# Kernel optimization log

Measured on AMD Instinct MI355X. Metric: run time of the kernel, lower is better.

Reference implementation:

```python
import jax, jax.numpy as jnp
import numpy as np

B, N, DIM = 32, 1024, 768
H, S, D = 16, 4, 64  # num_heads, num_subheads (L=H*S=64), attn_dim


def setup_inputs() -> dict:
    key = jax.random.key(0)
    k1, k2, k3, k4 = jax.random.split(key, 4)
    x = jax.random.normal(k1, (B, N, DIM), dtype=jnp.float32)
    eos_indices = jax.random.randint(k2, (B,), 0, N)
    # q_emb: original shape (1,H,S,1,D); singleton dims dropped -> (H,S,D)
    q_emb = jax.random.normal(k3, (H, S, D), dtype=jnp.float32)
    # k Linear(dim -> H*D), xavier-uniform weight, zero bias (share_kv: v == k)
    limit = float(np.sqrt(6.0 / (DIM + H * D)))
    Wk = jax.random.uniform(k4, (DIM, H * D), dtype=jnp.float32, minval=-limit, maxval=limit)
    bk = jnp.zeros((H * D,), dtype=jnp.float32)
    return {"x": x, "eos_indices": eos_indices, "q_emb": q_emb, "Wk": Wk, "bk": bk}


def reference(x, eos_indices, q_emb, Wk, bk):
    # x: (B,N,dim); shared k/v projection -> (B,N,H,D)
    kv = (x @ Wk + bk).reshape(x.shape[0], x.shape[1], H, D)
    scale = D ** -0.5
    # Avoid the torch expand over subheads: contract directly.
    # logits: (B,H,S,N)
    logits = jnp.einsum("hsd,bnhd->bhsn", q_emb * scale, kv)
    # eos masking: positions strictly after eos index are masked out
    mask = jnp.arange(x.shape[1])[None, None, None, :] > eos_indices[:, None, None, None]
    logits = jnp.where(mask, -jnp.inf, logits)
    attn = jax.nn.softmax(logits, axis=-1)
    # weighted sum over N -> (B,H,S,D) -> (B,L,D)
    out = jnp.einsum("bhsn,bnhd->bhsd", attn, kv)
    return out.reshape(x.shape[0], H * S, D)
```

## Files before the change

kernel.cpp:

```cpp
#include <hip/hip_runtime.h>
#include <hip/hip_bf16.h>
#include <stdint.h>

typedef float  f32x4  __attribute__((ext_vector_type(4)));
typedef __bf16 bf16x4 __attribute__((ext_vector_type(4)));
typedef __bf16 bf16x8 __attribute__((ext_vector_type(8)));
typedef unsigned int u32x2 __attribute__((ext_vector_type(2)));
typedef unsigned int u32x4 __attribute__((ext_vector_type(4)));

#define AS1 __attribute__((address_space(1)))
#define AS3 __attribute__((address_space(3)))

__device__ __forceinline__ void async_load16(const void* g, void* lds) {
    __builtin_amdgcn_global_load_lds((const AS1 unsigned int*)g,
                                     (AS3 unsigned int*)lds, 16, 0, 0);
}

__global__ __launch_bounds__(256) void qw_kernel(const float* __restrict__ q_emb,
                                                 const float* __restrict__ wk,
                                                 __bf16* __restrict__ qwT) {
    __shared__ float qlds[256];
    __shared__ float part[4096];
    const int t = threadIdx.x;
    const int kc = blockIdx.x;
    const int h  = blockIdx.y;
    const int k0 = kc * 64;
    qlds[t] = q_emb[h * 256 + t] * 0.125f;
    __syncthreads();
    const int dseg = t & 15;
    const int krow = t >> 4;
#pragma unroll
    for (int i = 0; i < 4; ++i) {
        const int k = i * 16 + krow;
        f32x4 wv = *(const f32x4*)&wk[(size_t)(k0 + k) * 1024 + h * 64 + dseg * 4];
#pragma unroll
        for (int s = 0; s < 4; ++s) {
            float p = qlds[s * 64 + dseg * 4 + 0] * wv[0]
                    + qlds[s * 64 + dseg * 4 + 1] * wv[1]
                    + qlds[s * 64 + dseg * 4 + 2] * wv[2]
                    + qlds[s * 64 + dseg * 4 + 3] * wv[3];
            part[k * 64 + s * 16 + dseg] = p;
        }
    }
    __syncthreads();
    const int k = t >> 2, s = t & 3;
    const float* pp = &part[k * 64 + s * 16];
    float sum = 0.f;
#pragma unroll
    for (int j = 0; j < 16; ++j) sum += pp[j];
    qwT[(h * 4 + s) * 768 + k0 + k] = (__bf16)sum;
}

__global__ __launch_bounds__(512) void logits_kernel(const float* __restrict__ x,
                                                     const __bf16* __restrict__ qwT,
                                                     float* __restrict__ Lg) {
    __shared__ char smem[49152];
    char* Bl = smem;
    char* Al = smem + 16384;
    const int t = threadIdx.x, l = t & 63, w = t >> 6;
    const int m0 = blockIdx.x * 128;
    const int bb = m0 >> 10, n0 = m0 & 1023;
    const int wrA = (w >> 1) * 32;
    const int wcB = (w & 1) * 32;

    f32x4 acc[2][2];
#pragma unroll
    for (int i = 0; i < 2; ++i)
#pragma unroll
        for (int j = 0; j < 2; ++j) acc[i][j] = (f32x4)0.f;

    const int Bcol = t >> 3, Bseg = t & 7;
    const __bf16* qsrc = qwT + Bcol * 768 + (Bseg ^ (Bcol & 7)) * 8;
    const int Arow0 = t >> 4;
    const int Aseg = t & 15;

    f32x4 av[4];
    async_load16(qsrc, Bl + t * 16);
#pragma unroll
    for (int i = 0; i < 4; ++i)
        av[i] = *(const f32x4*)&x[(size_t)(m0 + i * 32 + Arow0) * 768 + Aseg * 4];
#pragma unroll
    for (int i = 0; i < 4; ++i) {
        const int row = i * 32 + Arow0;
        bf16x4 vv = {(__bf16)av[i][0], (__bf16)av[i][1], (__bf16)av[i][2], (__bf16)av[i][3]};
        *(bf16x4*)(Al + ((row * 128 + Aseg * 8) ^ ((row & 7) << 4))) = vv;
    }
    asm volatile("s_waitcnt vmcnt(0)" ::: "memory");
    __syncthreads();

    int buf = 0;
    for (int step = 0; step < 12; ++step) {
        const int nbuf = buf ^ 1;
        const bool more = (step + 1) < 12;
        if (more) {
            const int kt = (step + 1) * 64;
            async_load16(qsrc + kt, Bl + nbuf * 8192 + t * 16);
#pragma unroll
            for (int i = 0; i < 4; ++i)
                av[i] = *(const f32x4*)&x[(size_t)(m0 + i * 32 + Arow0) * 768 + kt + Aseg * 4];
        }
#pragma unroll
        for (int kh = 0; kh < 2; ++kh) {
            const int u = kh * 4 + (l >> 4);
            bf16x8 af[2], bfr[2];
#pragma unroll
            for (int i = 0; i < 2; ++i) {
                const int row = wrA + i * 16 + (l & 15);
                af[i] = *(const bf16x8*)(Al + buf * 16384 +
                                         ((row * 128 + u * 16) ^ ((row & 7) << 4)));
            }
#pragma unroll
            for (int j = 0; j < 2; ++j) {
                const int col = wcB + j * 16 + (l & 15);
                bfr[j] = *(const bf16x8*)(Bl + buf * 8192 +
                                          ((col * 128 + u * 16) ^ ((col & 7) << 4)));
            }
#pragma unroll
            for (int i = 0; i < 2; ++i)
#pragma unroll
                for (int j = 0; j < 2; ++j)
                    acc[i][j] = __builtin_amdgcn_mfma_f32_16x16x32_bf16(
                        af[i], bfr[j], acc[i][j], 0, 0, 0);
        }
        if (more) {
#pragma unroll
            for (int i = 0; i < 4; ++i) {
                const int row = i * 32 + Arow0;
                bf16x4 vv = {(__bf16)av[i][0], (__bf16)av[i][1], (__bf16)av[i][2], (__bf16)av[i][3]};
                *(bf16x4*)(Al + nbuf * 16384 + ((row * 128 + Aseg * 8) ^ ((row & 7) << 4))) = vv;
            }
        }
        asm volatile("s_waitcnt vmcnt(0)" ::: "memory");
        __syncthreads();
        buf = nbuf;
    }

#pragma unroll
    for (int i = 0; i < 2; ++i)
#pragma unroll
        for (int j = 0; j < 2; ++j) {
            const int hs = wcB + j * 16 + (l & 15);
            const int nb = wrA + i * 16 + (l >> 4) * 4;
            *(f32x4*)(smem + ((hs * 512 + nb * 4) ^ ((hs & 7) << 4))) = acc[i][j];
        }
    __syncthreads();
    const int hs = t >> 3;
#pragma unroll
    for (int i = 0; i < 4; ++i) {
        const int seg = (t & 7) + i * 8;
        f32x4 v = *(const f32x4*)(smem + ((hs * 512 + seg * 16) ^ ((hs & 7) << 4)));
        *(f32x4*)&Lg[(size_t)bb * 65536 + hs * 1024 + n0 + seg * 4] = v;
    }
}

__global__ __launch_bounds__(256) void softmax_kernel(const float* __restrict__ Lg,
                                                      const int* __restrict__ eos_idx,
                                                      __bf16* __restrict__ P) {
    const int t = threadIdx.x, l = t & 63, s = t >> 6;
    const int b = blockIdx.x >> 4, h = blockIdx.x & 15;
    const int eos = eos_idx[b];
    const size_t base = (size_t)(b * 64 + h * 4 + s) * 1024;
    f32x4 v[4];
    float mx = -INFINITY;
#pragma unroll
    for (int i = 0; i < 4; ++i) {
        v[i] = *(const f32x4*)&Lg[base + i * 256 + l * 4];
#pragma unroll
        for (int j = 0; j < 4; ++j) {
            if (i * 256 + l * 4 + j > eos) v[i][j] = -INFINITY;
            mx = fmaxf(mx, v[i][j]);
        }
    }
#pragma unroll
    for (int off = 32; off; off >>= 1) mx = fmaxf(mx, __shfl_xor(mx, off));
    float sum = 0.f;
#pragma unroll
    for (int i = 0; i < 4; ++i)
#pragma unroll
        for (int j = 0; j < 4; ++j) {
            const float p = __expf(v[i][j] - mx);
            v[i][j] = p;
            sum += p;
        }
#pragma unroll
    for (int off = 32; off; off >>= 1) sum += __shfl_xor(sum, off);
    const float inv = 1.0f / sum;
#pragma unroll
    for (int i = 0; i < 4; ++i) {
        bf16x4 pk = {(__bf16)(v[i][0] * inv), (__bf16)(v[i][1] * inv),
                     (__bf16)(v[i][2] * inv), (__bf16)(v[i][3] * inv)};
        *(bf16x4*)&P[base + i * 256 + l * 4] = pk;
    }
}

__global__ __launch_bounds__(256) void pv_kernel(const float* __restrict__ x,
                                                 const __bf16* __restrict__ P,
                                                 float* __restrict__ y) {
    __shared__ char smem[32768];
    char* Pl = smem;
    char* Xl = smem + 16384;
    const int t = threadIdx.x, l = t & 63, w = t >> 6;
    const int vid = (blockIdx.x & 7) * 48 + (blockIdx.x >> 3);
    const int b = vid / 12, kc = vid % 12;
    const int k0 = kc * 64;
    const int wrA = (w >> 1) * 32, wcB = (w & 1) * 32;
    const __bf16* Pb = P + (size_t)b * 65536;
    const float* xb = x + (size_t)b * 786432 + k0 + l;
    const int fK = ((l & 7) << 4) | (((l >> 3) & 1) << 3);

    f32x4 acc[2][2];
#pragma unroll
    for (int i = 0; i < 2; ++i)
#pragma unroll
        for (int j = 0; j < 2; ++j) acc[i][j] = (f32x4)0.f;

    const int Prow = t >> 3;
    const int Pseg = t & 7;

    float xv[16];
#pragma unroll
    for (int ii = 0; ii < 2; ++ii) {
        const int row = ii * 32 + Prow;
        async_load16(Pb + row * 1024 + (Pseg ^ (row & 7)) * 8, Pl + ii * 4096 + t * 16);
    }
#pragma unroll
    for (int i = 0; i < 4; ++i)
#pragma unroll
        for (int j = 0; j < 4; ++j)
            xv[i * 4 + j] = xb[(size_t)(i * 16 + w * 4 + j) * 768];
#pragma unroll
    for (int i = 0; i < 4; ++i) {
        bf16x4 vv = {(__bf16)xv[i * 4 + 0], (__bf16)xv[i * 4 + 1],
                     (__bf16)xv[i * 4 + 2], (__bf16)xv[i * 4 + 3]};
        const int nb2 = (i * 16 + w * 4) * 2;
        *(bf16x4*)(Xl + ((l * 128 + nb2) ^ fK)) = vv;
    }
    asm volatile("s_waitcnt vmcnt(0)" ::: "memory");
    __syncthreads();

    int buf = 0;
    for (int step = 0; step < 16; ++step) {
        const int nbuf = buf ^ 1;
        const bool more = (step + 1) < 16;
        if (more) {
            const int nt = (step + 1) * 64;
#pragma unroll
            for (int ii = 0; ii < 2; ++ii) {
                const int row = ii * 32 + Prow;
                async_load16(Pb + row * 1024 + nt + (Pseg ^ (row & 7)) * 8,
                             Pl + nbuf * 8192 + ii * 4096 + t * 16);
            }
#pragma unroll
            for (int i = 0; i < 4; ++i)
#pragma unroll
                for (int j = 0; j < 4; ++j)
                    xv[i * 4 + j] = xb[(size_t)(nt + i * 16 + w * 4 + j) * 768];
        }
#pragma unroll
        for (int kh = 0; kh < 2; ++kh) {
            const int u = kh * 4 + (l >> 4);
            bf16x8 af[2], bfr[2];
#pragma unroll
            for (int i = 0; i < 2; ++i) {
                const int row = wrA + i * 16 + (l & 15);
                af[i] = *(const bf16x8*)(Pl + buf * 8192 +
                                         ((row * 128 + u * 16) ^ ((row & 7) << 4)));
            }
#pragma unroll
            for (int j = 0; j < 2; ++j) {
                const int kcol = wcB + j * 16 + (l & 15);
                const int fKc = ((kcol & 7) << 4) | (((kcol >> 3) & 1) << 3);
                const int addrA = kcol * 128 + kh * 64 + (l >> 4) * 16;
                u32x2 lo = *(const u32x2*)(Xl + buf * 8192 + (addrA ^ fKc));
                u32x2 hi = *(const u32x2*)(Xl + buf * 8192 + ((addrA + 8) ^ fKc));
                u32x4 uu = {lo[0], lo[1], hi[0], hi[1]};
                bfr[j] = __builtin_bit_cast(bf16x8, uu);
            }
#pragma unroll
            for (int i = 0; i < 2; ++i)
#pragma unroll
                for (int j = 0; j < 2; ++j)
                    acc[i][j] = __builtin_amdgcn_mfma_f32_16x16x32_bf16(
                        af[i], bfr[j], acc[i][j], 0, 0, 0);
        }
        if (more) {
#pragma unroll
            for (int i = 0; i < 4; ++i) {
                bf16x4 vv = {(__bf16)xv[i * 4 + 0], (__bf16)xv[i * 4 + 1],
                             (__bf16)xv[i * 4 + 2], (__bf16)xv[i * 4 + 3]};
                const int nb2 = (i * 16 + w * 4) * 2;
                *(bf16x4*)(Xl + nbuf * 8192 + ((l * 128 + nb2) ^ fK)) = vv;
            }
        }
        asm volatile("s_waitcnt vmcnt(0)" ::: "memory");
        __syncthreads();
        buf = nbuf;
    }

#pragma unroll
    for (int i = 0; i < 2; ++i)
#pragma unroll
        for (int j = 0; j < 2; ++j) {
            const int kcol = wcB + j * 16 + (l & 15);
#pragma unroll
            for (int r = 0; r < 4; ++r) {
                const int hs = wrA + i * 16 + (l >> 4) * 4 + r;
                *(float*)(smem + ((hs * 256 + kcol * 4) ^ ((hs & 7) << 4))) = acc[i][j][r];
            }
        }
    __syncthreads();
    const int hs2 = t >> 2;
#pragma unroll
    for (int i = 0; i < 4; ++i) {
        const int seg = (t & 3) + i * 4;
        f32x4 v = *(const f32x4*)(smem + ((hs2 * 256 + seg * 16) ^ ((hs2 & 7) << 4)));
        *(f32x4*)&y[(size_t)(b * 64 + hs2) * 768 + k0 + seg * 4] = v;
    }
}

__global__ __launch_bounds__(256) void out_kernel(const float* __restrict__ y,
                                                  const float* __restrict__ wk,
                                                  const float* __restrict__ bk,
                                                  float* __restrict__ out) {
    __shared__ float ylds[8 * 768];
    __shared__ float red[2048];
    const int t = threadIdx.x;
    const int vid = (blockIdx.x & 7) * 32 + (blockIdx.x >> 3);
    const int h = vid >> 4, bp = vid & 15;
#pragma unroll
    for (int r = 0; r < 8; ++r) {
        const int gb = bp * 2 + (r >> 2);
        const int hs = h * 4 + (r & 3);
#pragma unroll
        for (int i = 0; i < 3; ++i)
            ylds[r * 768 + i * 256 + t] = y[(size_t)(gb * 64 + hs) * 768 + i * 256 + t];
    }
    __syncthreads();
    const int kp = t >> 6, d = t & 63;
    float acc[8] = {0.f, 0.f, 0.f, 0.f, 0.f, 0.f, 0.f, 0.f};
    for (int i = 0; i < 48; ++i) {
        const int k = kp * 192 + i * 4;
        const float wv0 = wk[(size_t)(k + 0) * 1024 + h * 64 + d];
        const float wv1 = wk[(size_t)(k + 1) * 1024 + h * 64 + d];
        const float wv2 = wk[(size_t)(k + 2) * 1024 + h * 64 + d];
        const float wv3 = wk[(size_t)(k + 3) * 1024 + h * 64 + d];
#pragma unroll
        for (int r = 0; r < 8; ++r) {
            f32x4 yv = *(const f32x4*)&ylds[r * 768 + k];
            acc[r] += yv[0] * wv0 + yv[1] * wv1 + yv[2] * wv2 + yv[3] * wv3;
        }
    }
#pragma unroll
    for (int r = 0; r < 8; ++r) red[(r * 64 + d) * 4 + kp] = acc[r];
    __syncthreads();
#pragma unroll
    for (int i = 0; i < 2; ++i) {
        const int o = i * 256 + t;
        const int r = o >> 6, dd = o & 63;
        f32x4 pv = *(const f32x4*)&red[o * 4];
        const float s = pv[0] + pv[1] + pv[2] + pv[3] + bk[h * 64 + dd];
        const int gb = bp * 2 + (r >> 2);
        out[(size_t)(gb * 64 + h * 4 + (r & 3)) * 64 + dd] = s;
    }
}

extern "C" void kernel_launch(void* const* d_in, const int* in_sizes, int n_in,
                              void* d_out, int out_size, void* d_ws, size_t ws_size,
                              hipStream_t stream) {
    const float* x     = (const float*)d_in[0];
    const int*   eos   = (const int*)d_in[1];
    const float* q_emb = (const float*)d_in[2];
    const float* Wk    = (const float*)d_in[3];
    const float* bk    = (const float*)d_in[4];
    float* out = (float*)d_out;

    char* ws = (char*)d_ws;
    __bf16* qwT = (__bf16*)ws;
    float*  Lg  = (float*)(ws + 131072);
    __bf16* P   = (__bf16*)(ws + 131072 + 8388608);
    float*  y   = (float*)(ws + 131072 + 8388608 + 4194304);

    qw_kernel<<<dim3(12, 16), 256, 0, stream>>>(q_emb, Wk, qwT);
    logits_kernel<<<dim3(256), 512, 0, stream>>>(x, qwT, Lg);
    softmax_kernel<<<dim3(512), 256, 0, stream>>>(Lg, eos, P);
    pv_kernel<<<dim3(384), 256, 0, stream>>>(x, P, y);
    out_kernel<<<dim3(256), 256, 0, stream>>>(y, Wk, bk, out);
}
```

Measured before the change: 64.12 us.

## Fuse softmax into logits and PV kernels via split-softmax partial stats

Removes the standalone softmax kernel. The logits kernel now applies the eos mask and writes per-chunk max and sum-exp partials. The PV kernel combines these partials into a per-row max and inverse sum, then recomputes exp and normalisation on the fly as it loads the fp32 logits into LDS as bf16. This saves one launch and the P write/read round trip. In exchange PV now reads fp32 logits (twice the bytes of bf16 P) with synchronous loads in place of async global-to-LDS copies, and recomputes exponentials for each of the 12 column-chunk blocks.

```diff
diff --git a/kernel.cpp b/kernel.cpp
--- a/kernel.cpp
+++ b/kernel.cpp
@@ -53,13 +53,16 @@
 
 __global__ __launch_bounds__(512) void logits_kernel(const float* __restrict__ x,
                                                      const __bf16* __restrict__ qwT,
-                                                     float* __restrict__ Lg) {
+                                                     const int* __restrict__ eos_idx,
+                                                     float* __restrict__ Lg,
+                                                     float* __restrict__ partials) {
     __shared__ char smem[49152];
     char* Bl = smem;
     char* Al = smem + 16384;
     const int t = threadIdx.x, l = t & 63, w = t >> 6;
     const int m0 = blockIdx.x * 128;
     const int bb = m0 >> 10, n0 = m0 & 1023;
+    const int chunk = blockIdx.x & 7;
     const int wrA = (w >> 1) * 32;
     const int wcB = (w & 1) * 32;
 
@@ -144,57 +147,42 @@
             *(f32x4*)(smem + ((hs * 512 + nb * 4) ^ ((hs & 7) << 4))) = acc[i][j];
         }
     __syncthreads();
+    const int eosb = eos_idx[bb];
     const int hs = t >> 3;
+    f32x4 vv[4];
+    float mx = -INFINITY;
 #pragma unroll
     for (int i = 0; i < 4; ++i) {
         const int seg = (t & 7) + i * 8;
         f32x4 v = *(const f32x4*)(smem + ((hs * 512 + seg * 16) ^ ((hs & 7) << 4)));
+#pragma unroll
+        for (int j = 0; j < 4; ++j) {
+            if (n0 + seg * 4 + j > eosb) v[j] = -INFINITY;
+            mx = fmaxf(mx, v[j]);
+        }
+        vv[i] = v;
         *(f32x4*)&Lg[(size_t)bb * 65536 + hs * 1024 + n0 + seg * 4] = v;
     }
-}
-
-__global__ __launch_bounds__(256) void softmax_kernel(const float* __restrict__ Lg,
-                                                      const int* __restrict__ eos_idx,
-                                                      __bf16* __restrict__ P) {
-    const int t = threadIdx.x, l = t & 63, s = t >> 6;
-    const int b = blockIdx.x >> 4, h = blockIdx.x & 15;
-    const int eos = eos_idx[b];
-    const size_t base = (size_t)(b * 64 + h * 4 + s) * 1024;
-    f32x4 v[4];
-    float mx = -INFINITY;
-#pragma unroll
-    for (int i = 0; i < 4; ++i) {
-        v[i] = *(const f32x4*)&Lg[base + i * 256 + l * 4];
-#pragma unroll
-        for (int j = 0; j < 4; ++j) {
-            if (i * 256 + l * 4 + j > eos) v[i][j] = -INFINITY;
-            mx = fmaxf(mx, v[i][j]);
-        }
-    }
-#pragma unroll
-    for (int off = 32; off; off >>= 1) mx = fmaxf(mx, __shfl_xor(mx, off));
-    float sum = 0.f;
-#pragma unroll
-    for (int i = 0; i < 4; ++i)
-#pragma unroll
-        for (int j = 0; j < 4; ++j) {
-            const float p = __expf(v[i][j] - mx);
-            v[i][j] = p;
-            sum += p;
-        }
-#pragma unroll
-    for (int off = 32; off; off >>= 1) sum += __shfl_xor(sum, off);
-    const float inv = 1.0f / sum;
-#pragma unroll
-    for (int i = 0; i < 4; ++i) {
-        bf16x4 pk = {(__bf16)(v[i][0] * inv), (__bf16)(v[i][1] * inv),
-                     (__bf16)(v[i][2] * inv), (__bf16)(v[i][3] * inv)};
-        *(bf16x4*)&P[base + i * 256 + l * 4] = pk;
+#pragma unroll
+    for (int off = 1; off < 8; off <<= 1) mx = fmaxf(mx, __shfl_xor(mx, off));
+    float sl = 0.f;
+    if (mx > -INFINITY) {
+#pragma unroll
+        for (int i = 0; i < 4; ++i)
+#pragma unroll
+            for (int j = 0; j < 4; ++j) sl += __expf(vv[i][j] - mx);
+    }
+#pragma unroll
+    for (int off = 1; off < 8; off <<= 1) sl += __shfl_xor(sl, off);
+    if ((t & 7) == 0) {
+        float2 st = {mx, sl};
+        *(float2*)&partials[(size_t)(((bb * 8 + chunk) * 64) + hs) * 2] = st;
     }
 }
 
 __global__ __launch_bounds__(256) void pv_kernel(const float* __restrict__ x,
-                                                 const __bf16* __restrict__ P,
+                                                 const float* __restrict__ Lg,
+                                                 const float* __restrict__ partials,
                                                  float* __restrict__ y) {
     __shared__ char smem[32768];
     char* Pl = smem;
@@ -204,24 +192,54 @@
     const int b = vid / 12, kc = vid % 12;
     const int k0 = kc * 64;
     const int wrA = (w >> 1) * 32, wcB = (w & 1) * 32;
-    const __bf16* Pb = P + (size_t)b * 65536;
+    const float* Lgb = Lg + (size_t)b * 65536;
     const float* xb = x + (size_t)b * 786432 + k0 + l;
     const int fK = ((l & 7) << 4) | (((l >> 3) & 1) << 3);
 
+    const int r0 = t >> 3, r1 = 32 + (t >> 3);
+    float m0r, i0r, m1r, i1r;
+    {
+        const float* pb = partials + (size_t)b * 1024;
+        float m = -INFINITY, m2 = -INFINITY;
+#pragma unroll
+        for (int c = 0; c < 8; ++c) {
+            m  = fmaxf(m,  pb[(c * 64 + r0) * 2]);
+            m2 = fmaxf(m2, pb[(c * 64 + r1) * 2]);
+        }
+        float s = 0.f, s2 = 0.f;
+#pragma unroll
+        for (int c = 0; c < 8; ++c) {
+            float2 p0 = *(const float2*)&pb[(c * 64 + r0) * 2];
+            float2 p1 = *(const float2*)&pb[(c * 64 + r1) * 2];
+            s  += p0.y * __expf(p0.x - m);
+            s2 += p1.y * __expf(p1.x - m2);
+        }
+        m0r = m; i0r = 1.0f / s;
+        m1r = m2; i1r = 1.0f / s2;
+    }
+    const int n0s0 = (((t & 7) ^ (r0 & 7)) * 8);
+    const int n0s1 = (((t & 7) ^ (r1 & 7)) * 8);
+
     f32x4 acc[2][2];
 #pragma unroll
     for (int i = 0; i < 2; ++i)
 #pragma unroll
         for (int j = 0; j < 2; ++j) acc[i][j] = (f32x4)0.f;
 
-    const int Prow = t >> 3;
-    const int Pseg = t & 7;
-
     float xv[16];
 #pragma unroll
     for (int ii = 0; ii < 2; ++ii) {
-        const int row = ii * 32 + Prow;
-        async_load16(Pb + row * 1024 + (Pseg ^ (row & 7)) * 8, Pl + ii * 4096 + t * 16);
+        const int r = ii ? r1 : r0;
+        const int ns = ii ? n0s1 : n0s0;
+        const float mr = ii ? m1r : m0r, ir = ii ? i1r : i0r;
+        f32x4 lo = *(const f32x4*)&Lgb[(size_t)r * 1024 + ns];
+        f32x4 hi = *(const f32x4*)&Lgb[(size_t)r * 1024 + ns + 4];
+        bf16x8 pk;
+#pragma unroll
+        for (int j = 0; j < 4; ++j) pk[j]     = (__bf16)(__expf(lo[j] - mr) * ir);
+#pragma unroll
+        for (int j = 0; j < 4; ++j) pk[4 + j] = (__bf16)(__expf(hi[j] - mr) * ir);
+        *(bf16x8*)(Pl + ii * 4096 + t * 16) = pk;
     }
 #pragma unroll
     for (int i = 0; i < 4; ++i)
@@ -235,7 +253,6 @@
         const int nb2 = (i * 16 + w * 4) * 2;
         *(bf16x4*)(Xl + ((l * 128 + nb2) ^ fK)) = vv;
     }
-    asm volatile("s_waitcnt vmcnt(0)" ::: "memory");
     __syncthreads();
 
     int buf = 0;
@@ -246,9 +263,17 @@
             const int nt = (step + 1) * 64;
 #pragma unroll
             for (int ii = 0; ii < 2; ++ii) {
-                const int row = ii * 32 + Prow;
-                async_load16(Pb + row * 1024 + nt + (Pseg ^ (row & 7)) * 8,
-                             Pl + nbuf * 8192 + ii * 4096 + t * 16);
+                const int r = ii ? r1 : r0;
+                const int ns = ii ? n0s1 : n0s0;
+                const float mr = ii ? m1r : m0r, ir = ii ? i1r : i0r;
+                f32x4 lo = *(const f32x4*)&Lgb[(size_t)r * 1024 + nt + ns];
+                f32x4 hi = *(const f32x4*)&Lgb[(size_t)r * 1024 + nt + ns + 4];
+                bf16x8 pk;
+#pragma unroll
+                for (int j = 0; j < 4; ++j) pk[j]     = (__bf16)(__expf(lo[j] - mr) * ir);
+#pragma unroll
+                for (int j = 0; j < 4; ++j) pk[4 + j] = (__bf16)(__expf(hi[j] - mr) * ir);
+                *(bf16x8*)(Pl + nbuf * 8192 + ii * 4096 + t * 16) = pk;
             }
 #pragma unroll
             for (int i = 0; i < 4; ++i)
@@ -292,7 +317,6 @@
                 *(bf16x4*)(Xl + nbuf * 8192 + ((l * 128 + nb2) ^ fK)) = vv;
             }
         }
-        asm volatile("s_waitcnt vmcnt(0)" ::: "memory");
         __syncthreads();
         buf = nbuf;
     }
@@ -304,8 +328,8 @@
             const int kcol = wcB + j * 16 + (l & 15);
 #pragma unroll
             for (int r = 0; r < 4; ++r) {
-                const int hs = wrA + i * 16 + (l >> 4) * 4 + r;
-                *(float*)(smem + ((hs * 256 + kcol * 4) ^ ((hs & 7) << 4))) = acc[i][j][r];
+                const int hs2 = wrA + i * 16 + (l >> 4) * 4 + r;
+                *(float*)(smem + ((hs2 * 256 + kcol * 4) ^ ((hs2 & 7) << 4))) = acc[i][j][r];
             }
         }
     __syncthreads();
@@ -375,14 +399,13 @@
     float* out = (float*)d_out;
 
     char* ws = (char*)d_ws;
-    __bf16* qwT = (__bf16*)ws;
-    float*  Lg  = (float*)(ws + 131072);
-    __bf16* P   = (__bf16*)(ws + 131072 + 8388608);
-    float*  y   = (float*)(ws + 131072 + 8388608 + 4194304);
+    __bf16* qwT      = (__bf16*)ws;
+    float*  Lg       = (float*)(ws + 131072);
+    float*  partials = (float*)(ws + 131072 + 8388608);
+    float*  y        = (float*)(ws + 131072 + 8388608 + 131072);
 
     qw_kernel<<<dim3(12, 16), 256, 0, stream>>>(q_emb, Wk, qwT);
-    logits_kernel<<<dim3(256), 512, 0, stream>>>(x, qwT, Lg);
-    softmax_kernel<<<dim3(512), 256, 0, stream>>>(Lg, eos, P);
-    pv_kernel<<<dim3(384), 256, 0, stream>>>(x, P, y);
+    logits_kernel<<<dim3(256), 512, 0, stream>>>(x, qwT, eos, Lg, partials);
+    pv_kernel<<<dim3(384), 256, 0, stream>>>(x, Lg, partials, y);
     out_kernel<<<dim3(256), 256, 0, stream>>>(y, Wk, bk, out);
 }
```

New measurement: 63.83 us. About the same (-0.4%).
